# Optimization experiments

Hardware: AMD Instinct MI355X
Metric: run time of the kernel (lower is better)

The kernel has to match this reference:

```python
import jax, jax.numpy as jnp
import numpy as np

NEG_SLOPE = 0.2  # PyG GATConv default negative_slope


def gat_conv(x, edge_index, W, att_src, att_dst, bias):
    """PyG-style GATConv (concat heads, add_self_loops=True, eval mode).
    x: [N, F_in], edge_index: [2, E] (row 0 = src j, row 1 = dst i).
    W: [F_in, H*C], att_src/att_dst: [H, C], bias: [H*C].
    """
    N = x.shape[0]
    H, C = att_src.shape
    loops = jnp.arange(N, dtype=edge_index.dtype)
    src = jnp.concatenate([edge_index[0], loops])  # [E+N]
    dst = jnp.concatenate([edge_index[1], loops])
    h = (x @ W).reshape(N, H, C)                              # [N,H,C]
    a_src = jnp.einsum('nhc,hc->nh', h, att_src)              # [N,H]
    a_dst = jnp.einsum('nhc,hc->nh', h, att_dst)
    alpha = jax.nn.leaky_relu(a_src[src] + a_dst[dst], NEG_SLOPE)  # [E+N,H]
    # segment softmax over edges sharing the same destination node
    m = jax.ops.segment_max(alpha, dst, num_segments=N)       # [N,H]
    e = jnp.exp(alpha - jax.lax.stop_gradient(m)[dst])
    denom = jax.ops.segment_sum(e, dst, num_segments=N)       # [N,H]
    a = e / (denom[dst] + 1e-16)                              # [E+N,H]
    msg = h[src] * a[:, :, None]                              # [E+N,H,C]
    out = jax.ops.segment_sum(msg, dst, num_segments=N)       # [N,H,C]
    return out.reshape(N, H * C) + bias


def setup_inputs() -> dict:
    key = jax.random.key(0)
    ks = jax.random.split(key, 10)
    N, F, NC, C1, H1 = 50000, 128, 40, 16, 8
    E = 800000
    x = jax.random.normal(ks[0], (N, F), dtype=jnp.float32)
    edge_index = jax.random.randint(ks[1], (2, E), 0, N, dtype=jnp.int64)
    s1 = 1.0 / np.sqrt(F)
    W1 = jax.random.uniform(ks[2], (F, H1 * C1), jnp.float32, -s1, s1)
    att_src1 = jax.random.uniform(ks[3], (H1, C1), jnp.float32, -1.0, 1.0) * s1
    att_dst1 = jax.random.uniform(ks[4], (H1, C1), jnp.float32, -1.0, 1.0) * s1
    bias1 = jnp.zeros((H1 * C1,), jnp.float32)
    s2 = 1.0 / np.sqrt(H1 * C1)
    W2 = jax.random.uniform(ks[5], (H1 * C1, NC), jnp.float32, -s2, s2)
    att_src2 = jax.random.uniform(ks[6], (1, NC), jnp.float32, -1.0, 1.0) * s2
    att_dst2 = jax.random.uniform(ks[7], (1, NC), jnp.float32, -1.0, 1.0) * s2
    bias2 = jnp.zeros((NC,), jnp.float32)
    return {"x": x, "edge_index": edge_index, "W1": W1, "att_src1": att_src1,
            "att_dst1": att_dst1, "bias1": bias1, "W2": W2, "att_src2": att_src2,
            "att_dst2": att_dst2, "bias2": bias2}


def reference(x, edge_index, W1, att_src1, att_dst1, bias1, W2, att_src2, att_dst2, bias2):
    h = gat_conv(x, edge_index, W1, att_src1, att_dst1, bias1)   # [N, 128]
    # dropout in eval mode = identity
    out = gat_conv(h, edge_index, W2, att_src2, att_dst2, bias2)  # [N, 40]
    return out
```

## Files before the change

### kernel.cpp

```cpp
#include <hip/hip_runtime.h>
#include <hip/hip_bf16.h>
#include <math.h>

#define NEG_SLOPE 0.2f

typedef __bf16 bf16x8 __attribute__((ext_vector_type(8)));
typedef float f32x4 __attribute__((ext_vector_type(4)));

__device__ __forceinline__ float lrelu(float x) { return x > 0.f ? x : NEG_SLOPE * x; }

__device__ __forceinline__ unsigned short f2bfu(float f) {
    unsigned int ua = __float_as_uint(f);
    return (unsigned short)((ua + 0x7fffu + ((ua >> 16) & 1u)) >> 16);
}
__device__ __forceinline__ float bfu2f(unsigned short u) {
    return __uint_as_float(((unsigned int)u) << 16);
}
__device__ __forceinline__ float bf_lo(unsigned int u) { return __uint_as_float(u << 16); }
__device__ __forceinline__ float bf_hi(unsigned int u) { return __uint_as_float(u & 0xffff0000u); }

__global__ __launch_bounds__(256) void k_prep(const float* __restrict__ W1,
                                              bf16x8* __restrict__ Wp,
                                              const float* __restrict__ W2,
                                              bf16x8* __restrict__ W2p,
                                              int* __restrict__ cnt, int N) {
    int g = blockIdx.x * 256 + threadIdx.x;
    if (g < 2048) {
        int n = g & 15, quad = (g >> 4) & 3, c = (g >> 6) & 3, ct = g >> 8;
        bf16x8 v;
#pragma unroll
        for (int j = 0; j < 8; ++j)
            v[j] = (__bf16)W1[(c * 32 + quad * 8 + j) * 128 + ct * 16 + n];
        Wp[g] = v;
    } else if (g < 2816) {
        int idx = g - 2048;
        int n = idx & 15, quad = (idx >> 4) & 3, c = (idx >> 6) & 3, ct = idx >> 8;
        int colc = ct * 16 + n;
        bf16x8 v;
#pragma unroll
        for (int j = 0; j < 8; ++j)
            v[j] = (colc < 40) ? (__bf16)W2[(c * 32 + quad * 8 + j) * 40 + colc] : (__bf16)0.f;
        W2p[idx] = v;
    }
    if (g < N) cnt[g] = 0;
}

__global__ __launch_bounds__(256) void k_hist(const int* __restrict__ ei, int E, int N,
                                              int* __restrict__ cnt,
                                              unsigned short* __restrict__ rank) {
    int e = blockIdx.x * 256 + threadIdx.x;
    if (e >= E + N) return;
    int d = (e < E) ? ei[E + e] : (e - E);
    rank[e] = (unsigned short)atomicAdd(&cnt[d], 1);
}

__global__ __launch_bounds__(256) void k_scan_part(const int* __restrict__ cnt, int N,
                                                   int* __restrict__ psum) {
    __shared__ int sh[256];
    int t = threadIdx.x;
    int base = blockIdx.x * 1024 + t * 4;
    int tl = 0;
#pragma unroll
    for (int j = 0; j < 4; ++j) tl += (base + j < N) ? cnt[base + j] : 0;
    sh[t] = tl; __syncthreads();
    for (int off = 128; off > 0; off >>= 1) {
        if (t < off) sh[t] += sh[t + off];
        __syncthreads();
    }
    if (t == 0) psum[blockIdx.x] = sh[0];
}

__global__ __launch_bounds__(256) void k_scan_add(const int* __restrict__ cnt, int N,
                                                  const int* __restrict__ psum,
                                                  int* __restrict__ rowptr) {
    __shared__ int sh[256];
    __shared__ int basep;
    int t = threadIdx.x;
    if (t == 0) {
        int s = 0;
        for (int i = 0; i < blockIdx.x; ++i) s += psum[i];
        basep = s;
    }
    int base = blockIdx.x * 1024 + t * 4;
    int c[4]; int tl = 0;
#pragma unroll
    for (int j = 0; j < 4; ++j) { c[j] = (base + j < N) ? cnt[base + j] : 0; tl += c[j]; }
    sh[t] = tl; __syncthreads();
    for (int off = 1; off < 256; off <<= 1) {
        int a = (t >= off) ? sh[t - off] : 0;
        __syncthreads();
        sh[t] += a;
        __syncthreads();
    }
    int run = basep + (sh[t] - tl);
#pragma unroll
    for (int j = 0; j < 4; ++j) {
        if (base + j < N) { rowptr[base + j] = run; run += c[j]; }
    }
}

__global__ __launch_bounds__(256) void k_scatter_ev(const int* __restrict__ ei, int E, int N,
                                                    const int* __restrict__ rowptr,
                                                    const unsigned short* __restrict__ rank,
                                                    unsigned short* __restrict__ col,
                                                    const float* __restrict__ a_src,
                                                    const float* __restrict__ a_dst,
                                                    float* __restrict__ evA,
                                                    float* __restrict__ evB) {
    int e = blockIdx.x * 256 + threadIdx.x;
    if (e >= E + N) return;
    int s, d;
    if (e < E) { s = ei[e]; d = ei[E + e]; } else { s = d = e - E; }
    int slot = rowptr[d] + (int)rank[e];
    col[slot] = (unsigned short)s;
    float4 asA = *(const float4*)&a_src[(size_t)s * 8];
    float4 asB = *(const float4*)&a_src[(size_t)s * 8 + 4];
    float4 adA = *(const float4*)&a_dst[(size_t)d * 8];
    float4 adB = *(const float4*)&a_dst[(size_t)d * 8 + 4];
    float4 eA = make_float4(__expf(lrelu(asA.x + adA.x)), __expf(lrelu(asA.y + adA.y)),
                            __expf(lrelu(asA.z + adA.z)), __expf(lrelu(asA.w + adA.w)));
    float4 eB = make_float4(__expf(lrelu(asB.x + adB.x)), __expf(lrelu(asB.y + adB.y)),
                            __expf(lrelu(asB.z + adB.z)), __expf(lrelu(asB.w + adB.w)));
    *(float4*)&evA[(size_t)slot * 4] = eA;
    *(float4*)&evB[(size_t)slot * 4] = eB;
}

__global__ __launch_bounds__(256) void k_gemm1(const float* __restrict__ x,
                                               const bf16x8* __restrict__ Wp,
                                               const float* __restrict__ att_s,
                                               const float* __restrict__ att_d,
                                               unsigned short* __restrict__ h1A,
                                               unsigned short* __restrict__ h1B,
                                               float* __restrict__ a_src,
                                               float* __restrict__ a_dst, int N) {
    int t = threadIdx.x;
    int w = t >> 6, lane = t & 63, quad = lane >> 4, n16 = lane & 15;
    int row0 = blockIdx.x * 64 + w * 16;
    int arow = row0 + n16; if (arow >= N) arow = N - 1;
    const float* px = x + (size_t)arow * 128;

    bf16x8 ah[4], al[4];
#pragma unroll
    for (int c = 0; c < 4; ++c) {
        float4 v0 = *(const float4*)&px[c * 32 + quad * 8];
        float4 v1 = *(const float4*)&px[c * 32 + quad * 8 + 4];
        float xf[8] = {v0.x, v0.y, v0.z, v0.w, v1.x, v1.y, v1.z, v1.w};
#pragma unroll
        for (int j = 0; j < 8; ++j) {
            __bf16 hi = (__bf16)xf[j];
            ah[c][j] = hi;
            al[c][j] = (__bf16)(xf[j] - (float)hi);
        }
    }

    f32x4 acc[8];
#pragma unroll
    for (int ct = 0; ct < 8; ++ct) acc[ct] = (f32x4){0.f, 0.f, 0.f, 0.f};

    const uint4* wp4 = (const uint4*)Wp;
#pragma unroll
    for (int ct = 0; ct < 8; ++ct) {
#pragma unroll
        for (int c = 0; c < 4; ++c) {
            union { uint4 u; bf16x8 b; } bu;
            bu.u = wp4[((ct * 4 + c) * 4 + quad) * 16 + n16];
            acc[ct] = __builtin_amdgcn_mfma_f32_16x16x32_bf16(ah[c], bu.b, acc[ct], 0, 0, 0);
            acc[ct] = __builtin_amdgcn_mfma_f32_16x16x32_bf16(al[c], bu.b, acc[ct], 0, 0, 0);
        }
    }

    float asv[8], adv[8];
#pragma unroll
    for (int ct = 0; ct < 8; ++ct) {
        asv[ct] = att_s[ct * 16 + n16];
        adv[ct] = att_d[ct * 16 + n16];
    }
    int nodeb = row0 + quad * 4;
#pragma unroll
    for (int ct = 0; ct < 8; ++ct) {
        unsigned short* hp = (ct < 4) ? h1A : h1B;
        int chl = (ct & 3) * 16 + n16;
#pragma unroll
        for (int reg = 0; reg < 4; ++reg) {
            int node = nodeb + reg;
            float hv = acc[ct][reg];
            float ps = hv * asv[ct];
            float pd = hv * adv[ct];
#pragma unroll
            for (int m = 1; m < 16; m <<= 1) {
                ps += __shfl_xor(ps, m);
                pd += __shfl_xor(pd, m);
            }
            if (node < N) {
                hp[(size_t)node * 64 + chl] = f2bfu(hv);
                if (n16 == 0) {
                    a_src[(size_t)node * 8 + ct] = ps;
                    a_dst[(size_t)node * 8 + ct] = pd;
                }
            }
        }
    }
}

__global__ __launch_bounds__(256) void k_aggr1(const int* __restrict__ rowptr,
                                               const int* __restrict__ cnt,
                                               const unsigned short* __restrict__ col,
                                               const float* __restrict__ evA,
                                               const float* __restrict__ evB,
                                               const unsigned int* __restrict__ h1A,
                                               const unsigned int* __restrict__ h1B,
                                               const float* __restrict__ bias1,
                                               unsigned int* __restrict__ out1h,
                                               unsigned int* __restrict__ out1l,
                                               int N, int nag) {
    __shared__ float evs[4][2][128];
    __shared__ int   cls[4][2][32];
    int p = (blockIdx.x >= nag) ? 1 : 0;
    int blk = blockIdx.x - p * nag;
    const uint4* hp4 = (const uint4*)(p ? h1B : h1A);
    const float4* evp = (const float4*)(p ? evB : evA);
    int t = threadIdx.x;
    int w = t >> 6;
    int lane = t & 63;
    int half = lane >> 5;
    int u = lane & 31;
    int e4 = u >> 3;
    int v  = u & 7;
    int hh = v >> 1;
    int node = blk * 8 + w * 2 + half;
    bool nv = (node < N);
    int nodec = nv ? node : (N - 1);
    int beg = rowptr[nodec];
    int deg = nv ? cnt[nodec] : 0;
    int degO = __shfl_xor(deg, 32);
    int degmax = (deg > degO) ? deg : degO;
    if (degmax <= 0) return;

    float* myev = &evs[w][half][0];
    int*   mycl = &cls[w][half][0];

    float den = 0.f;
    float nm[8];
#pragma unroll
    for (int k = 0; k < 8; ++k) nm[k] = 0.f;

    int c = 0;
    while (c < degmax) {
        int slot = c + u;
        int slotc = (slot < deg) ? slot : (deg - 1);
        if (slotc < 0) slotc = 0;
        int su = (int)col[beg + slotc];
        float4 e4v = evp[beg + slotc];
        if (slot >= deg) e4v = make_float4(0.f, 0.f, 0.f, 0.f);
        *(float4*)&myev[u * 4] = e4v;
        mycl[u] = su;

        int ccm = degmax - c; ccm = (ccm < 32) ? ccm : 32;
        int ng = (ccm + 3) >> 2;
        int gl = ng - 1;
        int g1 = (1 < gl) ? 1 : gl;
        int g2 = (2 < gl) ? 2 : gl;
        int g3 = (3 < gl) ? 3 : gl;
        uint4 U0 = hp4[mycl[e4] * 8 + v];
        uint4 U1 = hp4[mycl[g1 * 4 + e4] * 8 + v];
        uint4 U2 = hp4[mycl[g2 * 4 + e4] * 8 + v];
        uint4 U3 = hp4[mycl[g3 * 4 + e4] * 8 + v];
        int body = ng - 4;
        int g = 0;
#pragma unroll 2
        for (; g < body; ++g) {
            uint4 UN = hp4[mycl[(g + 4) * 4 + e4] * 8 + v];
            float ev = myev[(g * 4 + e4) * 4 + hh];
            den += ev;
            nm[0] = fmaf(ev, bf_lo(U0.x), nm[0]);
            nm[1] = fmaf(ev, bf_hi(U0.x), nm[1]);
            nm[2] = fmaf(ev, bf_lo(U0.y), nm[2]);
            nm[3] = fmaf(ev, bf_hi(U0.y), nm[3]);
            nm[4] = fmaf(ev, bf_lo(U0.z), nm[4]);
            nm[5] = fmaf(ev, bf_hi(U0.z), nm[5]);
            nm[6] = fmaf(ev, bf_lo(U0.w), nm[6]);
            nm[7] = fmaf(ev, bf_hi(U0.w), nm[7]);
            U0 = U1; U1 = U2; U2 = U3; U3 = UN;
        }
        for (; g < ng; ++g) {
            float ev = myev[(g * 4 + e4) * 4 + hh];
            den += ev;
            nm[0] = fmaf(ev, bf_lo(U0.x), nm[0]);
            nm[1] = fmaf(ev, bf_hi(U0.x), nm[1]);
            nm[2] = fmaf(ev, bf_lo(U0.y), nm[2]);
            nm[3] = fmaf(ev, bf_hi(U0.y), nm[3]);
            nm[4] = fmaf(ev, bf_lo(U0.z), nm[4]);
            nm[5] = fmaf(ev, bf_hi(U0.z), nm[5]);
            nm[6] = fmaf(ev, bf_lo(U0.w), nm[6]);
            nm[7] = fmaf(ev, bf_hi(U0.w), nm[7]);
            U0 = U1; U1 = U2; U2 = U3;
        }
        c += 32;
    }
    den += __shfl_xor(den, 8);
    den += __shfl_xor(den, 16);
#pragma unroll
    for (int k = 0; k < 8; ++k) {
        nm[k] += __shfl_xor(nm[k], 8);
        nm[k] += __shfl_xor(nm[k], 16);
    }
    if (nv && e4 == 0) {
        float inv = 1.f / (den + 1e-16f);
        float4 b0 = *(const float4*)&bias1[p * 64 + v * 8];
        float4 b1 = *(const float4*)&bias1[p * 64 + v * 8 + 4];
        float bb[8] = {b0.x, b0.y, b0.z, b0.w, b1.x, b1.y, b1.z, b1.w};
        unsigned int H[4], L[4];
#pragma unroll
        for (int q = 0; q < 4; ++q) {
            float o0 = fmaf(nm[2 * q],     inv, bb[2 * q]);
            float o1 = fmaf(nm[2 * q + 1], inv, bb[2 * q + 1]);
            unsigned short h0 = f2bfu(o0), h1 = f2bfu(o1);
            float l0 = o0 - bfu2f(h0), l1 = o1 - bfu2f(h1);
            H[q] = (unsigned int)h0 | ((unsigned int)h1 << 16);
            L[q] = (unsigned int)f2bfu(l0) | ((unsigned int)f2bfu(l1) << 16);
        }
        size_t idx = (size_t)node * 64 + p * 32 + v * 4;
        *(uint4*)&out1h[idx] = make_uint4(H[0], H[1], H[2], H[3]);
        *(uint4*)&out1l[idx] = make_uint4(L[0], L[1], L[2], L[3]);
    }
}

__global__ __launch_bounds__(256) void k_gemm2(const unsigned int* __restrict__ out1h,
                                               const unsigned int* __restrict__ out1l,
                                               const bf16x8* __restrict__ W2p,
                                               const float* __restrict__ att_s2,
                                               const float* __restrict__ att_d2,
                                               unsigned short* __restrict__ h2s,
                                               float* __restrict__ a_src2,
                                               float* __restrict__ a_dst2, int N) {
    int t = threadIdx.x;
    int w = t >> 6, lane = t & 63, quad = lane >> 4, n16 = lane & 15;
    int row0 = blockIdx.x * 64 + w * 16;
    int arow = row0 + n16; if (arow >= N) arow = N - 1;

    bf16x8 ah[4], al[4];
#pragma unroll
    for (int c = 0; c < 4; ++c) {
        size_t base = (size_t)arow * 64 + (c * 32 + quad * 8) / 2;
        union { uint4 u; bf16x8 b; } hu, lu;
        hu.u = *(const uint4*)&out1h[base];
        lu.u = *(const uint4*)&out1l[base];
        ah[c] = hu.b;
        al[c] = lu.b;
    }

    f32x4 acc[3];
#pragma unroll
    for (int ct = 0; ct < 3; ++ct) acc[ct] = (f32x4){0.f, 0.f, 0.f, 0.f};

    const uint4* wp4 = (const uint4*)W2p;
#pragma unroll
    for (int ct = 0; ct < 3; ++ct) {
#pragma unroll
        for (int c = 0; c < 4; ++c) {
            union { uint4 u; bf16x8 b; } bu;
            bu.u = wp4[((ct * 4 + c) * 4 + quad) * 16 + n16];
            acc[ct] = __builtin_amdgcn_mfma_f32_16x16x32_bf16(ah[c], bu.b, acc[ct], 0, 0, 0);
            acc[ct] = __builtin_amdgcn_mfma_f32_16x16x32_bf16(al[c], bu.b, acc[ct], 0, 0, 0);
        }
    }

    float asv[3], adv[3];
#pragma unroll
    for (int ct = 0; ct < 3; ++ct) {
        int ch = ct * 16 + n16;
        asv[ct] = (ch < 40) ? att_s2[ch] : 0.f;
        adv[ct] = (ch < 40) ? att_d2[ch] : 0.f;
    }
    int nodeb = row0 + quad * 4;
#pragma unroll
    for (int reg = 0; reg < 4; ++reg) {
        int node = nodeb + reg;
        float ps = 0.f, pd = 0.f;
#pragma unroll
        for (int ct = 0; ct < 3; ++ct) {
            float hv = acc[ct][reg];
            ps = fmaf(hv, asv[ct], ps);
            pd = fmaf(hv, adv[ct], pd);
            int ch = ct * 16 + n16;
            if (node < N && ch < 40) h2s[(size_t)node * 64 + ch] = f2bfu(hv);
        }
#pragma unroll
        for (int m = 1; m < 16; m <<= 1) {
            ps += __shfl_xor(ps, m);
            pd += __shfl_xor(pd, m);
        }
        if (node < N && n16 == 0) {
            a_src2[node] = ps;
            a_dst2[node] = pd;
        }
    }
}

__global__ __launch_bounds__(256) void k_aggr2(const int* __restrict__ rowptr,
                                               const int* __restrict__ cnt,
                                               const unsigned short* __restrict__ col,
                                               const float* __restrict__ a_src,
                                               const float* __restrict__ a_dst,
                                               const unsigned int* __restrict__ h2b,
                                               const float* __restrict__ bias2,
                                               float* __restrict__ out, int N) {
    __shared__ float evs[4][2][32];
    __shared__ int   cls[4][2][32];
    int t = threadIdx.x;
    int w = t >> 6;
    int lane = t & 63;
    int half = lane >> 5;
    int u = lane & 31;
    int e4 = u >> 3;
    int v  = u & 7;
    int node = blockIdx.x * 8 + w * 2 + half;
    bool nv = (node < N);
    int nodec = nv ? node : (N - 1);
    int beg = rowptr[nodec];
    int deg = nv ? cnt[nodec] : 0;
    int degO = __shfl_xor(deg, 32);
    int degmax = (deg > degO) ? deg : degO;
    if (degmax <= 0) return;

    const uint4* h24 = (const uint4*)h2b;
    float ad = a_dst[nodec];
    float* myev = &evs[w][half][0];
    int*   mycl = &cls[w][half][0];

    float den = 0.f;
    float am[8];
#pragma unroll
    for (int k = 0; k < 8; ++k) am[k] = 0.f;

    int c = 0;
    while (c < degmax) {
        int slot = c + u;
        int slotc = (slot < deg) ? slot : (deg - 1);
        if (slotc < 0) slotc = 0;
        int su = (int)col[beg + slotc];
        float ev = (slot < deg) ? __expf(lrelu(a_src[su] + ad)) : 0.f;
        myev[u] = ev;
        mycl[u] = su;

        int ccm = degmax - c; ccm = (ccm < 32) ? ccm : 32;
        int ng = (ccm + 3) >> 2;
        int gl = ng - 1;
        int g1 = (1 < gl) ? 1 : gl;
        int g2 = (2 < gl) ? 2 : gl;
        int g3 = (3 < gl) ? 3 : gl;
        uint4 U0 = h24[mycl[e4] * 8 + v];
        uint4 U1 = h24[mycl[g1 * 4 + e4] * 8 + v];
        uint4 U2 = h24[mycl[g2 * 4 + e4] * 8 + v];
        uint4 U3 = h24[mycl[g3 * 4 + e4] * 8 + v];
        int body = ng - 4;
        int g = 0;
#pragma unroll 2
        for (; g < body; ++g) {
            uint4 UN = h24[mycl[(g + 4) * 4 + e4] * 8 + v];
            float evv = myev[g * 4 + e4];
            den += evv;
            am[0] = fmaf(evv, bf_lo(U0.x), am[0]);
            am[1] = fmaf(evv, bf_hi(U0.x), am[1]);
            am[2] = fmaf(evv, bf_lo(U0.y), am[2]);
            am[3] = fmaf(evv, bf_hi(U0.y), am[3]);
            am[4] = fmaf(evv, bf_lo(U0.z), am[4]);
            am[5] = fmaf(evv, bf_hi(U0.z), am[5]);
            am[6] = fmaf(evv, bf_lo(U0.w), am[6]);
            am[7] = fmaf(evv, bf_hi(U0.w), am[7]);
            U0 = U1; U1 = U2; U2 = U3; U3 = UN;
        }
        for (; g < ng; ++g) {
            float evv = myev[g * 4 + e4];
            den += evv;
            am[0] = fmaf(evv, bf_lo(U0.x), am[0]);
            am[1] = fmaf(evv, bf_hi(U0.x), am[1]);
            am[2] = fmaf(evv, bf_lo(U0.y), am[2]);
            am[3] = fmaf(evv, bf_hi(U0.y), am[3]);
            am[4] = fmaf(evv, bf_lo(U0.z), am[4]);
            am[5] = fmaf(evv, bf_hi(U0.z), am[5]);
            am[6] = fmaf(evv, bf_lo(U0.w), am[6]);
            am[7] = fmaf(evv, bf_hi(U0.w), am[7]);
            U0 = U1; U1 = U2; U2 = U3;
        }
        c += 32;
    }
    den += __shfl_xor(den, 8);
    den += __shfl_xor(den, 16);
#pragma unroll
    for (int k = 0; k < 8; ++k) {
        am[k] += __shfl_xor(am[k], 8);
        am[k] += __shfl_xor(am[k], 16);
    }
    if (nv && e4 == 0 && v < 5) {
        float inv = 1.f / (den + 1e-16f);
        float4 b0 = *(const float4*)&bias2[v * 8];
        float4 b1 = *(const float4*)&bias2[v * 8 + 4];
        float4 o0 = make_float4(fmaf(am[0], inv, b0.x), fmaf(am[1], inv, b0.y),
                                fmaf(am[2], inv, b0.z), fmaf(am[3], inv, b0.w));
        float4 o1 = make_float4(fmaf(am[4], inv, b1.x), fmaf(am[5], inv, b1.y),
                                fmaf(am[6], inv, b1.z), fmaf(am[7], inv, b1.w));
        size_t ob = (size_t)node * 40 + v * 8;
        *(float4*)&out[ob] = o0;
        *(float4*)&out[ob + 4] = o1;
    }
}

extern "C" void kernel_launch(void* const* d_in, const int* in_sizes, int n_in,
                              void* d_out, int out_size, void* d_ws, size_t ws_size,
                              hipStream_t stream) {
    const float* x   = (const float*)d_in[0];
    const int*   ei  = (const int*)d_in[1];
    const float* W1  = (const float*)d_in[2];
    const float* as1 = (const float*)d_in[3];
    const float* ad1 = (const float*)d_in[4];
    const float* b1  = (const float*)d_in[5];
    const float* W2  = (const float*)d_in[6];
    const float* as2 = (const float*)d_in[7];
    const float* ad2 = (const float*)d_in[8];
    const float* b2  = (const float*)d_in[9];

    int N = in_sizes[0] / 128;
    int E = in_sizes[1] / 2;
    int EN = E + N;
    size_t Np = (size_t)((N + 3) & ~3);
    size_t ENp = ((size_t)EN + 3) & ~3;

    float* ws = (float*)d_ws;
    unsigned int* out1h = (unsigned int*)ws; ws += Np * 64;
    unsigned int* out1l = (unsigned int*)ws; ws += Np * 64;
    unsigned int* h1A = (unsigned int*)ws; ws += Np * 32;
    unsigned int* h1Bp = (unsigned int*)ws; ws += Np * 32;
    unsigned int* h2b = (unsigned int*)ws; ws += Np * 32;
    float* a_src1  = ws; ws += Np * 8;
    float* a_dst1  = ws; ws += Np * 8;
    float* a_src2v = ws; ws += Np;
    float* a_dst2v = ws; ws += Np;
    float* evA = ws; ws += ENp * 4;
    float* evB = ws; ws += ENp * 4;
    bf16x8* Wp  = (bf16x8*)ws; ws += 2048 * 4;
    bf16x8* W2p = (bf16x8*)ws; ws += 768 * 4;
    int* cnt    = (int*)ws; ws += Np;
    int* rowptr = (int*)ws; ws += Np;
    int* psum   = (int*)ws; ws += 256;
    unsigned short* col  = (unsigned short*)ws; ws += ENp / 2 + 4;
    unsigned short* rank = (unsigned short*)ws; ws += ENp / 2 + 4;

    int nb = (N + 1023) / 1024;
    int npre = (N > 2816 ? N : 2816);

    k_prep<<<(npre + 255) / 256, 256, 0, stream>>>(W1, Wp, W2, W2p, cnt, N);
    k_gemm1<<<(N + 63) / 64, 256, 0, stream>>>(x, Wp, as1, ad1,
                                               (unsigned short*)h1A, (unsigned short*)h1Bp,
                                               a_src1, a_dst1, N);
    k_hist<<<(EN + 255) / 256, 256, 0, stream>>>(ei, E, N, cnt, rank);
    k_scan_part<<<nb, 256, 0, stream>>>(cnt, N, psum);
    k_scan_add<<<nb, 256, 0, stream>>>(cnt, N, psum, rowptr);
    k_scatter_ev<<<(EN + 255) / 256, 256, 0, stream>>>(ei, E, N, rowptr, rank, col,
                                                       a_src1, a_dst1, evA, evB);

    int nag = (N + 7) / 8;
    k_aggr1<<<2 * nag, 256, 0, stream>>>(rowptr, cnt, col, evA, evB,
                                         h1A, h1Bp, b1, out1h, out1l, N, nag);
    k_gemm2<<<(N + 63) / 64, 256, 0, stream>>>(out1h, out1l, W2p, as2, ad2,
                                               (unsigned short*)h2b, a_src2v, a_dst2v, N);
    k_aggr2<<<nag, 256, 0, stream>>>(rowptr, cnt, col, a_src2v, a_dst2v, h2b, b2, (float*)d_out, N);
}
```

Measured before the change: 261.8 us.

## Fold attention vectors into weight GEMMs and precompute edge scores in CSR order

Precomputes W·att products (hi/lo bf16 split) as extra GEMM columns, so gemm1 and gemm2 produce a_src/a_dst directly instead of using shuffle reductions. Edge-score computation moves from the scatter kernel into new CSR-ordered kernels (ev1 with a binary search over rowptr, ev2 for layer 2). aggr2 then reads precomputed exp scores rather than gathering a_src. This adds two launches, a binary search per edge, and extra ev2/d16 buffers.

After: 245.2 us. -6.3%, faster.

```diff
diff --git a/kernel.cpp b/kernel.cpp
--- a/kernel.cpp
+++ b/kernel.cpp
@@ -23,6 +23,10 @@
                                               bf16x8* __restrict__ Wp,
                                               const float* __restrict__ W2,
                                               bf16x8* __restrict__ W2p,
+                                              const float* __restrict__ att_s1,
+                                              const float* __restrict__ att_d1,
+                                              const float* __restrict__ att_s2,
+                                              const float* __restrict__ att_d2,
                                               int* __restrict__ cnt, int N) {
     int g = blockIdx.x * 256 + threadIdx.x;
     if (g < 2048) {
@@ -32,14 +36,45 @@
         for (int j = 0; j < 8; ++j)
             v[j] = (__bf16)W1[(c * 32 + quad * 8 + j) * 128 + ct * 16 + n];
         Wp[g] = v;
-    } else if (g < 2816) {
+    } else if (g < 2560) {
         int idx = g - 2048;
+        int n = idx & 15, quad = (idx >> 4) & 3, c = (idx >> 6) & 3, t8 = idx >> 8;
+        int h = n & 7;
+        const float* av = (n < 8) ? att_s1 : att_d1;
+        bf16x8 vv;
+#pragma unroll
+        for (int j = 0; j < 8; ++j) {
+            int f = c * 32 + quad * 8 + j;
+            float full = 0.f;
+            for (int cc = 0; cc < 16; ++cc)
+                full += W1[f * 128 + h * 16 + cc] * av[h * 16 + cc];
+            __bf16 hi = (__bf16)full;
+            vv[j] = t8 ? (__bf16)(full - (float)hi) : hi;
+        }
+        Wp[g] = vv;
+    } else if (g < 3328) {
+        int idx = g - 2560;
         int n = idx & 15, quad = (idx >> 4) & 3, c = (idx >> 6) & 3, ct = idx >> 8;
         int colc = ct * 16 + n;
         bf16x8 v;
-#pragma unroll
-        for (int j = 0; j < 8; ++j)
-            v[j] = (colc < 40) ? (__bf16)W2[(c * 32 + quad * 8 + j) * 40 + colc] : (__bf16)0.f;
+        if (colc < 40) {
+#pragma unroll
+            for (int j = 0; j < 8; ++j)
+                v[j] = (__bf16)W2[(c * 32 + quad * 8 + j) * 40 + colc];
+        } else if (ct == 2 && n >= 8 && n < 12) {
+            const float* av = (n & 1) ? att_d2 : att_s2;
+#pragma unroll
+            for (int j = 0; j < 8; ++j) {
+                int f = c * 32 + quad * 8 + j;
+                float full = 0.f;
+                for (int cc = 0; cc < 40; ++cc) full += W2[f * 40 + cc] * av[cc];
+                __bf16 hi = (__bf16)full;
+                v[j] = (n >= 10) ? (__bf16)(full - (float)hi) : hi;
+            }
+        } else {
+#pragma unroll
+            for (int j = 0; j < 8; ++j) v[j] = (__bf16)0.f;
+        }
         W2p[idx] = v;
     }
     if (g < N) cnt[g] = 0;
@@ -99,20 +134,35 @@
     }
 }
 
-__global__ __launch_bounds__(256) void k_scatter_ev(const int* __restrict__ ei, int E, int N,
-                                                    const int* __restrict__ rowptr,
-                                                    const unsigned short* __restrict__ rank,
-                                                    unsigned short* __restrict__ col,
-                                                    const float* __restrict__ a_src,
-                                                    const float* __restrict__ a_dst,
-                                                    float* __restrict__ evA,
-                                                    float* __restrict__ evB) {
+__global__ __launch_bounds__(256) void k_scatter(const int* __restrict__ ei, int E, int N,
+                                                 const int* __restrict__ rowptr,
+                                                 const unsigned short* __restrict__ rank,
+                                                 unsigned short* __restrict__ col) {
     int e = blockIdx.x * 256 + threadIdx.x;
     if (e >= E + N) return;
     int s, d;
     if (e < E) { s = ei[e]; d = ei[E + e]; } else { s = d = e - E; }
-    int slot = rowptr[d] + (int)rank[e];
-    col[slot] = (unsigned short)s;
+    col[rowptr[d] + (int)rank[e]] = (unsigned short)s;
+}
+
+__global__ __launch_bounds__(256) void k_ev1(const int* __restrict__ rowptr,
+                                             const unsigned short* __restrict__ col,
+                                             const float* __restrict__ a_src,
+                                             const float* __restrict__ a_dst,
+                                             float* __restrict__ evA,
+                                             float* __restrict__ evB,
+                                             unsigned short* __restrict__ d16,
+                                             int N, int EN) {
+    int slot = blockIdx.x * 256 + threadIdx.x;
+    if (slot >= EN) return;
+    int lo = 0, hi = N - 1;
+    while (lo < hi) {
+        int mid = (lo + hi + 1) >> 1;
+        if (rowptr[mid] <= slot) lo = mid; else hi = mid - 1;
+    }
+    int d = lo;
+    int s = (int)col[slot];
+    d16[slot] = (unsigned short)d;
     float4 asA = *(const float4*)&a_src[(size_t)s * 8];
     float4 asB = *(const float4*)&a_src[(size_t)s * 8 + 4];
     float4 adA = *(const float4*)&a_dst[(size_t)d * 8];
@@ -125,10 +175,20 @@
     *(float4*)&evB[(size_t)slot * 4] = eB;
 }
 
+__global__ __launch_bounds__(256) void k_ev2(const unsigned short* __restrict__ col,
+                                             const unsigned short* __restrict__ d16,
+                                             const float* __restrict__ a_src2,
+                                             const float* __restrict__ a_dst2,
+                                             float* __restrict__ ev2, int EN) {
+    int slot = blockIdx.x * 256 + threadIdx.x;
+    if (slot >= EN) return;
+    int s = (int)col[slot];
+    int d = (int)d16[slot];
+    ev2[slot] = __expf(lrelu(a_src2[s] + a_dst2[d]));
+}
+
 __global__ __launch_bounds__(256) void k_gemm1(const float* __restrict__ x,
                                                const bf16x8* __restrict__ Wp,
-                                               const float* __restrict__ att_s,
-                                               const float* __restrict__ att_d,
                                                unsigned short* __restrict__ h1A,
                                                unsigned short* __restrict__ h1B,
                                                float* __restrict__ a_src,
@@ -153,13 +213,13 @@
         }
     }
 
-    f32x4 acc[8];
-#pragma unroll
-    for (int ct = 0; ct < 8; ++ct) acc[ct] = (f32x4){0.f, 0.f, 0.f, 0.f};
+    f32x4 acc[10];
+#pragma unroll
+    for (int ct = 0; ct < 10; ++ct) acc[ct] = (f32x4){0.f, 0.f, 0.f, 0.f};
 
     const uint4* wp4 = (const uint4*)Wp;
 #pragma unroll
-    for (int ct = 0; ct < 8; ++ct) {
+    for (int ct = 0; ct < 10; ++ct) {
 #pragma unroll
         for (int c = 0; c < 4; ++c) {
             union { uint4 u; bf16x8 b; } bu;
@@ -169,12 +229,6 @@
         }
     }
 
-    float asv[8], adv[8];
-#pragma unroll
-    for (int ct = 0; ct < 8; ++ct) {
-        asv[ct] = att_s[ct * 16 + n16];
-        adv[ct] = att_d[ct * 16 + n16];
-    }
     int nodeb = row0 + quad * 4;
 #pragma unroll
     for (int ct = 0; ct < 8; ++ct) {
@@ -183,21 +237,16 @@
 #pragma unroll
         for (int reg = 0; reg < 4; ++reg) {
             int node = nodeb + reg;
-            float hv = acc[ct][reg];
-            float ps = hv * asv[ct];
-            float pd = hv * adv[ct];
-#pragma unroll
-            for (int m = 1; m < 16; m <<= 1) {
-                ps += __shfl_xor(ps, m);
-                pd += __shfl_xor(pd, m);
-            }
-            if (node < N) {
-                hp[(size_t)node * 64 + chl] = f2bfu(hv);
-                if (n16 == 0) {
-                    a_src[(size_t)node * 8 + ct] = ps;
-                    a_dst[(size_t)node * 8 + ct] = pd;
-                }
-            }
+            if (node < N) hp[(size_t)node * 64 + chl] = f2bfu(acc[ct][reg]);
+        }
+    }
+#pragma unroll
+    for (int reg = 0; reg < 4; ++reg) {
+        int node = nodeb + reg;
+        float av = acc[8][reg] + acc[9][reg];
+        if (node < N) {
+            if (n16 < 8) a_src[(size_t)node * 8 + n16] = av;
+            else         a_dst[(size_t)node * 8 + (n16 - 8)] = av;
         }
     }
 }
@@ -328,8 +377,6 @@
 __global__ __launch_bounds__(256) void k_gemm2(const unsigned int* __restrict__ out1h,
                                                const unsigned int* __restrict__ out1l,
                                                const bf16x8* __restrict__ W2p,
-                                               const float* __restrict__ att_s2,
-                                               const float* __restrict__ att_d2,
                                                unsigned short* __restrict__ h2s,
                                                float* __restrict__ a_src2,
                                                float* __restrict__ a_dst2, int N) {
@@ -365,34 +412,20 @@
         }
     }
 
-    float asv[3], adv[3];
-#pragma unroll
-    for (int ct = 0; ct < 3; ++ct) {
-        int ch = ct * 16 + n16;
-        asv[ct] = (ch < 40) ? att_s2[ch] : 0.f;
-        adv[ct] = (ch < 40) ? att_d2[ch] : 0.f;
-    }
     int nodeb = row0 + quad * 4;
 #pragma unroll
     for (int reg = 0; reg < 4; ++reg) {
         int node = nodeb + reg;
-        float ps = 0.f, pd = 0.f;
 #pragma unroll
         for (int ct = 0; ct < 3; ++ct) {
-            float hv = acc[ct][reg];
-            ps = fmaf(hv, asv[ct], ps);
-            pd = fmaf(hv, adv[ct], pd);
             int ch = ct * 16 + n16;
-            if (node < N && ch < 40) h2s[(size_t)node * 64 + ch] = f2bfu(hv);
-        }
-#pragma unroll
-        for (int m = 1; m < 16; m <<= 1) {
-            ps += __shfl_xor(ps, m);
-            pd += __shfl_xor(pd, m);
-        }
-        if (node < N && n16 == 0) {
-            a_src2[node] = ps;
-            a_dst2[node] = pd;
+            if (node < N && ch < 40) h2s[(size_t)node * 64 + ch] = f2bfu(acc[ct][reg]);
+        }
+        float fv = acc[2][reg];
+        float fused = fv + __shfl_xor(fv, 2);
+        if (node < N) {
+            if (n16 == 8) a_src2[node] = fused;
+            else if (n16 == 9) a_dst2[node] = fused;
         }
     }
 }
@@ -400,8 +433,7 @@
 __global__ __launch_bounds__(256) void k_aggr2(const int* __restrict__ rowptr,
                                                const int* __restrict__ cnt,
                                                const unsigned short* __restrict__ col,
-                                               const float* __restrict__ a_src,
-                                               const float* __restrict__ a_dst,
+                                               const float* __restrict__ ev2,
                                                const unsigned int* __restrict__ h2b,
                                                const float* __restrict__ bias2,
                                                float* __restrict__ out, int N) {
@@ -424,7 +456,6 @@
     if (degmax <= 0) return;
 
     const uint4* h24 = (const uint4*)h2b;
-    float ad = a_dst[nodec];
     float* myev = &evs[w][half][0];
     int*   mycl = &cls[w][half][0];
 
@@ -439,7 +470,8 @@
         int slotc = (slot < deg) ? slot : (deg - 1);
         if (slotc < 0) slotc = 0;
         int su = (int)col[beg + slotc];
-        float ev = (slot < deg) ? __expf(lrelu(a_src[su] + ad)) : 0.f;
+        float ev = ev2[beg + slotc];
+        if (slot >= deg) ev = 0.f;
         myev[u] = ev;
         mycl[u] = su;
 
@@ -538,31 +570,36 @@
     float* a_dst2v = ws; ws += Np;
     float* evA = ws; ws += ENp * 4;
     float* evB = ws; ws += ENp * 4;
-    bf16x8* Wp  = (bf16x8*)ws; ws += 2048 * 4;
+    float* ev2 = ws; ws += ENp;
+    bf16x8* Wp  = (bf16x8*)ws; ws += 2560 * 4;
     bf16x8* W2p = (bf16x8*)ws; ws += 768 * 4;
     int* cnt    = (int*)ws; ws += Np;
     int* rowptr = (int*)ws; ws += Np;
     int* psum   = (int*)ws; ws += 256;
     unsigned short* col  = (unsigned short*)ws; ws += ENp / 2 + 4;
     unsigned short* rank = (unsigned short*)ws; ws += ENp / 2 + 4;
+    unsigned short* d16  = (unsigned short*)ws; ws += ENp / 2 + 4;
 
     int nb = (N + 1023) / 1024;
-    int npre = (N > 2816 ? N : 2816);
-
-    k_prep<<<(npre + 255) / 256, 256, 0, stream>>>(W1, Wp, W2, W2p, cnt, N);
-    k_gemm1<<<(N + 63) / 64, 256, 0, stream>>>(x, Wp, as1, ad1,
-                                               (unsigned short*)h1A, (unsigned short*)h1Bp,
-                                               a_src1, a_dst1, N);
+    int npre = (N > 3328 ? N : 3328);
+
+    k_prep<<<(npre + 255) / 256, 256, 0, stream>>>(W1, Wp, W2, W2p,
+                                                   as1, ad1, as2, ad2, cnt, N);
     k_hist<<<(EN + 255) / 256, 256, 0, stream>>>(ei, E, N, cnt, rank);
     k_scan_part<<<nb, 256, 0, stream>>>(cnt, N, psum);
     k_scan_add<<<nb, 256, 0, stream>>>(cnt, N, psum, rowptr);
-    k_scatter_ev<<<(EN + 255) / 256, 256, 0, stream>>>(ei, E, N, rowptr, rank, col,
-                                                       a_src1, a_dst1, evA, evB);
-
+    k_scatter<<<(EN + 255) / 256, 256, 0, stream>>>(ei, E, N, rowptr, rank, col);
+
+    k_gemm1<<<(N + 63) / 64, 256, 0, stream>>>(x, Wp,
+                                               (unsigned short*)h1A, (unsigned short*)h1Bp,
+                                               a_src1, a_dst1, N);
+    k_ev1<<<(EN + 255) / 256, 256, 0, stream>>>(rowptr, col, a_src1, a_dst1,
+                                                evA, evB, d16, N, EN);
     int nag = (N + 7) / 8;
     k_aggr1<<<2 * nag, 256, 0, stream>>>(rowptr, cnt, col, evA, evB,
                                          h1A, h1Bp, b1, out1h, out1l, N, nag);
-    k_gemm2<<<(N + 63) / 64, 256, 0, stream>>>(out1h, out1l, W2p, as2, ad2,
+    k_gemm2<<<(N + 63) / 64, 256, 0, stream>>>(out1h, out1l, W2p,
                                                (unsigned short*)h2b, a_src2v, a_dst2v, N);
-    k_aggr2<<<nag, 256, 0, stream>>>(rowptr, cnt, col, a_src2v, a_dst2v, h2b, b2, (float*)d_out, N);
-}
+    k_ev2<<<(EN + 255) / 256, 256, 0, stream>>>(col, d16, a_src2v, a_dst2v, ev2, EN);
+    k_aggr2<<<nag, 256, 0, stream>>>(rowptr, cnt, col, ev2, h2b, b2, (float*)d_out, N);
+}
```
